# Performance work log

Measured on AMD Instinct MI355X. Metric: run time of the kernel, lower is better.

## Reference

```python
import jax, jax.numpy as jnp
import numpy as np

N_NODES = 10000

def rgcn_layer(x, edge_index, basis, comp, root, bias):
    # x: [N, Fin]; edge_index: [R, 2, E] int; basis: [B, Fin, Fout]; comp: [R, B]
    R, _, E = edge_index.shape
    N = x.shape[0]
    src = edge_index[:, 0]  # [R, E]
    dst = edge_index[:, 1]  # [R, E]
    # basis-decomposed per-relation weights: W_r = sum_b comp[r,b] * basis[b]
    W = jnp.einsum('rb,bio->rio', comp, basis)          # [R, Fin, Fout]
    x_src = x[src]                                       # [R, E, Fin] gather
    msg = jnp.einsum('rei,rio->reo', x_src, W)           # [R, E, Fout]
    # per-relation mean aggregation onto destination nodes
    seg = (jnp.arange(R, dtype=dst.dtype)[:, None] * N + dst).reshape(-1)  # [R*E]
    agg = jax.ops.segment_sum(msg.reshape(R * E, -1), seg, num_segments=R * N)
    deg = jax.ops.segment_sum(jnp.ones((R * E,), x.dtype), seg, num_segments=R * N)
    agg = agg / jnp.maximum(deg, 1.0)[:, None]
    agg = agg.reshape(R, N, -1).sum(0)                   # sum over relations
    return agg + x @ root + bias


def setup_inputs() -> dict:
    key = jax.random.key(0)
    ks = jax.random.split(key, 10)
    s = 0.05  # scale params for numerical sanity
    return {
        'x_drug': jax.random.normal(ks[0], (N_NODES, 2048), jnp.float32),
        'drug_w': jax.random.normal(ks[1], (2048, 128), jnp.float32) * s,
        'edge_index': jax.random.randint(ks[2], (100, 2, 5000), 0, N_NODES, jnp.int32),
        'basis1': jax.random.normal(ks[3], (8, 128, 64), jnp.float32) * s,
        'comp1': jax.random.normal(ks[4], (100, 8), jnp.float32) * s,
        'root1': jax.random.normal(ks[5], (128, 64), jnp.float32) * s,
        'bias1': jnp.zeros((64,), jnp.float32),
        'basis2': jax.random.normal(ks[6], (8, 64, 20), jnp.float32) * s,
        'comp2': jax.random.normal(ks[7], (100, 8), jnp.float32) * s,
        'root2': jax.random.normal(ks[8], (64, 20), jnp.float32) * s,
        'bias2': jnp.zeros((20,), jnp.float32),
    }


def reference(x_drug, drug_w, edge_index, basis1, comp1, root1, bias1,
              basis2, comp2, root2, bias2):
    x = x_drug @ drug_w                                   # dense projection [N, 128]
    h = rgcn_layer(x, edge_index, basis1, comp1, root1, bias1)   # [N, 64]
    h = jax.nn.relu(h)
    out = rgcn_layer(h, edge_index, basis2, comp2, root2, bias2)  # [N, 20]
    return out
```

## Files before the change

### kernel.cpp

```cpp
#include <hip/hip_runtime.h>

#define NN 10000
#define RR 100
#define EE 5000
#define D0 2048
#define D1 128
#define D2 64
#define D3 20
#define NE (RR*EE)
#define MAXD 128

using short8  = __attribute__((ext_vector_type(8))) short;
using float4e = __attribute__((ext_vector_type(4))) float;

typedef const __attribute__((address_space(1))) void g_void;
typedef __attribute__((address_space(3))) void l_void;

__device__ __forceinline__ unsigned short f2bf(float f) {
  unsigned int u = __float_as_uint(f);
  unsigned int r = u + 0x7fffu + ((u >> 16) & 1u);
  return (unsigned short)(r >> 16);
}
__device__ __forceinline__ float bf2f(unsigned short u) {
  return __uint_as_float(((unsigned int)u) << 16);
}
__device__ __forceinline__ unsigned int pk2(float lo, float hi) {
  return ((unsigned int)f2bf(hi) << 16) | (unsigned int)f2bf(lo);
}

#define ZBLK 977
#define CURB 10
#define WTBLK 1024
#define W1BLK 288
#define W2BLK 72
__global__ __launch_bounds__(256) void prep_kernel(
    const float* __restrict__ W, const float* __restrict__ root1,
    const float* __restrict__ basis1, const float* __restrict__ root2,
    const float* __restrict__ basis2, int4* __restrict__ deg4,
    int4* __restrict__ cur4,
    unsigned short* __restrict__ Btw, unsigned short* __restrict__ Wc1T,
    unsigned short* __restrict__ Wc2T) {
  const int b = blockIdx.x, tid = threadIdx.x;
  if (b < ZBLK) {
    int i = b * 256 + tid;
    if (i < (NN * RR) / 4) deg4[i] = make_int4(0, 0, 0, 0);
  } else if (b < ZBLK + CURB) {
    int i = (b - ZBLK) * 256 + tid;
    if (i < 2504) cur4[i] = make_int4(0, 0, 0, 0);
  } else if (b < ZBLK + CURB + WTBLK) {
    int idx = (b - ZBLK - CURB) * 256 + tid;
    int n = idx >> 11, k = idx & 2047;
    Btw[idx] = f2bf(W[(size_t)k * 128 + n]);
  } else if (b < ZBLK + CURB + WTBLK + W1BLK) {
    int idx = (b - ZBLK - CURB - WTBLK) * 256 + tid;
    int o = idx / 1152, j = idx - o * 1152;
    float v = (j < 128) ? root1[j * 64 + o] : basis1[(j - 128) * 64 + o];
    Wc1T[idx] = f2bf(v);
  } else {
    int idx = (b - ZBLK - CURB - WTBLK - W1BLK) * 256 + tid;
    int c = idx / 576, j = idx - c * 576;
    float v = 0.f;
    if (c < 20) v = (j < 64) ? root2[j * 20 + c] : basis2[(j - 64) * 20 + c];
    Wc2T[idx] = f2bf(v);
  }
}

__global__ void deg_kernel(const int* __restrict__ ei, int* __restrict__ deg) {
  int gid = blockIdx.x * 256 + threadIdx.x;
  if (gid >= NE) return;
  int r = gid / EE, e = gid - r * EE;
  int d = ei[r * 2 * EE + EE + e];
  atomicAdd(&deg[r * NN + d], 1);
}

__global__ void scatter_kernel(const int* __restrict__ ei,
                               const int* __restrict__ deg,
                               int* __restrict__ cur, int* __restrict__ rec,
                               float* __restrict__ esc) {
  int gid = blockIdx.x * 256 + threadIdx.x;
  if (gid >= NE) return;
  int r = gid / EE, e = gid - r * EE;
  int s = ei[r * 2 * EE + e];
  int d = ei[r * 2 * EE + EE + e];
  int p = atomicAdd(&cur[d], 1);
  if (p < MAXD) {
    rec[d * MAXD + p] = (r << 14) | s;
    esc[d * MAXD + p] = 1.0f / fmaxf((float)deg[r * NN + d], 1.0f);
  }
}

__global__ __launch_bounds__(256) void gemm0_mfma(
    const float* __restrict__ A, const unsigned short* __restrict__ Btw,
    unsigned short* __restrict__ xb) {
  __shared__ __align__(16) unsigned short Asb[2][16 * 64];
  __shared__ __align__(16) unsigned short Bsb[2][128 * 64];
  const int tid = threadIdx.x;
  const int m0 = blockIdx.x * 16;
  const int wv = tid >> 6, lane = tid & 63;
  const int lrow = lane & 15, quad = lane >> 4;

  const int ar = tid >> 4, ag = tid & 15;
  const float* Ap = &A[(size_t)(m0 + ar) * D0 + ag * 4];
  const int aw = (ar * 128 + ((ag * 8) ^ ((ar & 7) << 4))) >> 1;

  const int rowB = wv * 32 + (lane >> 3);
  const int gch  = (lane & 7) ^ (lane >> 3);
  const unsigned short* BgBase = &Btw[(size_t)rowB * D0 + gch * 8];
  const int ldsB = wv * 2048;

  float4 a0;

#define G0_LOADB(buf, c)                                                     \
  { _Pragma("unroll")                                                        \
    for (int i = 0; i < 4; i++) {                                            \
      __builtin_amdgcn_global_load_lds(                                      \
          (g_void*)(BgBase + (size_t)i * 8 * D0 + (c) * 64),                 \
          (l_void*)&Bsb[buf][ldsB + i * 512], 16, 0, 0);                     \
    } }

#define G0_LOADA(c)  { a0 = *(const float4*)(Ap + (c) * 64); }

#define G0_STOREA(buf)                                                  \
  { uint2 p0;                                                           \
    p0.x = pk2(a0.x, a0.y); p0.y = pk2(a0.z, a0.w);                     \
    *(uint2*)&Asb[buf][aw] = p0; }

#define G0_COMPUTE(buf)                                                 \
  { const int aswz = (lrow & 7) << 4;                                   \
    _Pragma("unroll")                                                   \
    for (int kk = 0; kk < 2; kk++) {                                    \
      short8 af = *(const short8*)&Asb[buf][(lrow * 128 + ((quad * 16 + kk * 64) ^ aswz)) >> 1]; \
      _Pragma("unroll")                                                 \
      for (int nt = 0; nt < 2; nt++) {                                  \
        const int brow = wv * 32 + nt * 16 + lrow;                      \
        short8 bfr = *(const short8*)&Bsb[buf][(brow * 128 + ((quad * 16 + kk * 64) ^ ((brow & 7) << 4))) >> 1]; \
        acc[nt] = __builtin_amdgcn_mfma_f32_16x16x32_bf16(af, bfr, acc[nt], 0, 0, 0); \
      }                                                                 \
    } }

  float4e acc[2];
#pragma unroll
  for (int i = 0; i < 2; i++) { acc[i][0]=0.f; acc[i][1]=0.f; acc[i][2]=0.f; acc[i][3]=0.f; }

  G0_LOADB(0, 0);
  G0_LOADA(0);
  G0_STOREA(0);
  __syncthreads();

#pragma unroll 4
  for (int c = 0; c < 32; c++) {
    if (c < 31) {
      G0_LOADB((c + 1) & 1, c + 1);
      G0_LOADA(c + 1);
      __builtin_amdgcn_sched_barrier(0);
    }
    G0_COMPUTE(c & 1);
    if (c < 31) G0_STOREA((c + 1) & 1);
    __syncthreads();
  }

#pragma unroll
  for (int nt = 0; nt < 2; nt++) {
    const int col = wv * 32 + nt * 16 + lrow;
#pragma unroll
    for (int r = 0; r < 4; r++) {
      const int row = m0 + quad * 4 + r;
      xb[(size_t)row * D1 + col] = f2bf(acc[nt][r]);
    }
  }
}

__global__ __launch_bounds__(256) void agg1e_kernel(
    const unsigned short* __restrict__ xb, const int* __restrict__ cur,
    const int* __restrict__ rec, const float* __restrict__ esc,
    const float* __restrict__ comp, unsigned short* __restrict__ A1b) {
  __shared__ float s_comp[RR * 8];
  const int tid = threadIdx.x;
  for (int i = tid; i < RR * 8; i += 256) s_comp[i] = comp[i];
  __syncthreads();
  const int wv = tid >> 6, lane = tid & 63;
  const int n = blockIdx.x * 4 + wv;
  if (n >= NN) return;
  float acc[8][2];
#pragma unroll
  for (int b = 0; b < 8; b++) { acc[b][0] = 0.f; acc[b][1] = 0.f; }
  int cnt = cur[n]; if (cnt > MAXD) cnt = MAXD;
  const int beg = n * MAXD, end = beg + cnt;
  int idx = beg;
  for (; idx + 3 < end; idx += 4) {
    int rc[4]; float sc[4]; unsigned int xv[4];
#pragma unroll
    for (int u = 0; u < 4; u++) {
      rc[u] = rec[idx + u];
      sc[u] = esc[idx + u];
    }
#pragma unroll
    for (int u = 0; u < 4; u++)
      xv[u] = *(const unsigned int*)&xb[(size_t)(rc[u] & 16383) * D1 + lane * 2];
#pragma unroll
    for (int u = 0; u < 4; u++) {
      const float* cb = &s_comp[(rc[u] >> 14) * 8];
      float x0 = __uint_as_float((xv[u] & 0xffffu) << 16);
      float x1 = __uint_as_float(xv[u] & 0xffff0000u);
#pragma unroll
      for (int b = 0; b < 8; b++) {
        float w = sc[u] * cb[b];
        acc[b][0] += w * x0;
        acc[b][1] += w * x1;
      }
    }
  }
  for (; idx < end; idx++) {
    int rc = rec[idx];
    float sc = esc[idx];
    unsigned int xv = *(const unsigned int*)&xb[(size_t)(rc & 16383) * D1 + lane * 2];
    const float* cb = &s_comp[(rc >> 14) * 8];
    float x0 = __uint_as_float((xv & 0xffffu) << 16);
    float x1 = __uint_as_float(xv & 0xffff0000u);
#pragma unroll
    for (int b = 0; b < 8; b++) {
      float w = sc * cb[b];
      acc[b][0] += w * x0;
      acc[b][1] += w * x1;
    }
  }
#pragma unroll
  for (int b = 0; b < 8; b++) {
    ushort2 o; o.x = f2bf(acc[b][0]); o.y = f2bf(acc[b][1]);
    *(ushort2*)&A1b[(size_t)n * 1024 + b * 128 + lane * 2] = o;
  }
}

__global__ __launch_bounds__(256) void agg2e_kernel(
    const unsigned short* __restrict__ hb, const int* __restrict__ cur,
    const int* __restrict__ rec, const float* __restrict__ esc,
    const float* __restrict__ comp, unsigned short* __restrict__ A2b) {
  __shared__ float s_comp[RR * 8];
  const int tid = threadIdx.x;
  for (int i = tid; i < RR * 8; i += 256) s_comp[i] = comp[i];
  __syncthreads();
  const int wv = tid >> 6, lane = tid & 63;
  const int n = blockIdx.x * 4 + wv;
  if (n >= NN) return;
  float acc[8];
#pragma unroll
  for (int b = 0; b < 8; b++) acc[b] = 0.f;
  int cnt = cur[n]; if (cnt > MAXD) cnt = MAXD;
  const int beg = n * MAXD, end = beg + cnt;
  int idx = beg;
  for (; idx + 3 < end; idx += 4) {
    int rc[4]; float sc[4]; float hv[4];
#pragma unroll
    for (int u = 0; u < 4; u++) {
      rc[u] = rec[idx + u];
      sc[u] = esc[idx + u];
    }
#pragma unroll
    for (int u = 0; u < 4; u++)
      hv[u] = bf2f(hb[(size_t)(rc[u] & 16383) * D2 + lane]);
#pragma unroll
    for (int u = 0; u < 4; u++) {
      const float* cb = &s_comp[(rc[u] >> 14) * 8];
#pragma unroll
      for (int b = 0; b < 8; b++) acc[b] += sc[u] * cb[b] * hv[u];
    }
  }
  for (; idx < end; idx++) {
    int rc = rec[idx];
    float sc = esc[idx];
    float hv = bf2f(hb[(size_t)(rc & 16383) * D2 + lane]);
    const float* cb = &s_comp[(rc >> 14) * 8];
#pragma unroll
    for (int b = 0; b < 8; b++) acc[b] += sc * cb[b] * hv;
  }
#pragma unroll
  for (int b = 0; b < 8; b++)
    A2b[(size_t)n * 512 + b * 64 + lane] = f2bf(acc[b]);
}

__global__ __launch_bounds__(256) void hlayer_mfma(
    const unsigned short* __restrict__ xb, const unsigned short* __restrict__ A1b,
    const unsigned short* __restrict__ Wt, const float* __restrict__ bias1,
    unsigned short* __restrict__ hb) {
  __shared__ __align__(16) unsigned short Asb[2][32 * 64];
  __shared__ __align__(16) unsigned short Bsb[2][64 * 64];
  const int tid = threadIdx.x;
  const int m0 = blockIdx.x * 32;
  const int wv = tid >> 6, lane = tid & 63;
  const int lrow = lane & 15, quad = lane >> 4;
  const int mt = wv >> 1, nb = wv & 1;

  const int ar = tid >> 3, ac = tid & 7;
  int gr = m0 + ar; if (gr >= NN) gr = NN - 1;
  const unsigned short* Ax = &xb[(size_t)gr * D1 + ac * 8];
  const unsigned short* Aa = &A1b[(size_t)gr * 1024 + ac * 8];
  const int asw = (ar & 7) << 4;
  const int aw = (ar * 128 + ((ac * 16) ^ asw)) >> 1;

  const int br = tid >> 2, bq = tid & 3;
  const unsigned short* Bp = &Wt[(size_t)br * 1152 + bq * 16];
  const int bsw = (br & 7) << 4;
  const int bw0 = (br * 128 + ((bq * 32) ^ bsw)) >> 1;
  const int bw1 = (br * 128 + ((bq * 32 + 16) ^ bsw)) >> 1;

  uint4 ra, rb0, rb1;

#define H_LOADG(c)                                                       \
  { int kb = (c) * 64;                                                   \
    ra  = (kb < 128) ? *(const uint4*)(Ax + kb)                          \
                     : *(const uint4*)(Aa + (kb - 128));                 \
    rb0 = *(const uint4*)(Bp + kb);                                      \
    rb1 = *(const uint4*)(Bp + kb + 8); }

#define H_STOREL(buf)                                                    \
  { *(uint4*)&Asb[buf][aw]  = ra;                                        \
    *(uint4*)&Bsb[buf][bw0] = rb0;                                       \
    *(uint4*)&Bsb[buf][bw1] = rb1; }

#define H_COMPUTE(buf)                                                   \
  { const int arow = mt * 16 + lrow;                                     \
    const int aswz = (arow & 7) << 4;                                    \
    _Pragma("unroll")                                                    \
    for (int kk = 0; kk < 2; kk++) {                                     \
      short8 af = *(const short8*)&Asb[buf][(arow * 128 + ((quad * 16 + kk * 64) ^ aswz)) >> 1]; \
      _Pragma("unroll")                                                  \
      for (int nt = 0; nt < 2; nt++) {                                   \
        const int brow = nb * 32 + nt * 16 + lrow;                       \
        short8 bfr = *(const short8*)&Bsb[buf][(brow * 128 + ((quad * 16 + kk * 64) ^ ((brow & 7) << 4))) >> 1]; \
        acc[nt] = __builtin_amdgcn_mfma_f32_16x16x32_bf16(af, bfr, acc[nt], 0, 0, 0); \
      }                                                                  \
    } }

  float4e acc[2];
#pragma unroll
  for (int i = 0; i < 2; i++) { acc[i][0]=0.f; acc[i][1]=0.f; acc[i][2]=0.f; acc[i][3]=0.f; }

  H_LOADG(0);
  H_STOREL(0);
  __syncthreads();

#pragma unroll
  for (int c = 0; c < 18; c++) {
    if (c < 17) {
      H_LOADG(c + 1);
      __builtin_amdgcn_sched_barrier(0);
    }
    H_COMPUTE(c & 1);
    if (c < 17) H_STOREL((c + 1) & 1);
    __syncthreads();
  }

#pragma unroll
  for (int nt = 0; nt < 2; nt++) {
    int col = nb * 32 + nt * 16 + lrow;
    float bv = bias1[col];
#pragma unroll
    for (int r = 0; r < 4; r++) {
      int row = m0 + mt * 16 + quad * 4 + r;
      if (row < NN)
        hb[(size_t)row * D2 + col] = f2bf(fmaxf(acc[nt][r] + bv, 0.f));
    }
  }
}

__global__ __launch_bounds__(256) void out_mfma(
    const unsigned short* __restrict__ hb, const unsigned short* __restrict__ A2b,
    const unsigned short* __restrict__ Wt, const float* __restrict__ bias2,
    float* __restrict__ out) {
  __shared__ __align__(16) unsigned short Asb[2][32 * 64];
  __shared__ __align__(16) unsigned short Bsb[2][32 * 64];
  const int tid = threadIdx.x;
  const int m0 = blockIdx.x * 32;
  const int wv = tid >> 6, lane = tid & 63;
  const int lrow = lane & 15, quad = lane >> 4;
  const int mt = wv >> 1, ntn = wv & 1;

  const int ar = tid >> 3, ac = tid & 7;
  int gr = m0 + ar; if (gr >= NN) gr = NN - 1;
  const unsigned short* Ah = &hb[(size_t)gr * D2 + ac * 8];
  const unsigned short* Aa = &A2b[(size_t)gr * 512 + ac * 8];
  const unsigned short* Bp = &Wt[(size_t)ar * 576 + ac * 8];
  const int asw = (ar & 7) << 4;
  const int aw = (ar * 128 + ((ac * 16) ^ asw)) >> 1;

  uint4 ra, rb;

#define O_LOADG(c)                                                       \
  { int kb = (c) * 64;                                                   \
    ra = (kb < 64) ? *(const uint4*)(Ah)                                 \
                   : *(const uint4*)(Aa + (kb - 64));                    \
    rb = *(const uint4*)(Bp + kb); }

#define O_STOREL(buf)                                                    \
  { *(uint4*)&Asb[buf][aw] = ra;                                         \
    *(uint4*)&Bsb[buf][aw] = rb; }

#define O_COMPUTE(buf)                                                   \
  { const int arow = mt * 16 + lrow;                                     \
    const int aswz = (arow & 7) << 4;                                    \
    const int brow = ntn * 16 + lrow;                                    \
    const int bswz = (brow & 7) << 4;                                    \
    _Pragma("unroll")                                                    \
    for (int kk = 0; kk < 2; kk++) {                                     \
      short8 af = *(const short8*)&Asb[buf][(arow * 128 + ((quad * 16 + kk * 64) ^ aswz)) >> 1]; \
      short8 bfr = *(const short8*)&Bsb[buf][(brow * 128 + ((quad * 16 + kk * 64) ^ bswz)) >> 1]; \
      acc = __builtin_amdgcn_mfma_f32_16x16x32_bf16(af, bfr, acc, 0, 0, 0); \
    } }

  float4e acc;
  acc[0]=0.f; acc[1]=0.f; acc[2]=0.f; acc[3]=0.f;

  O_LOADG(0);
  O_STOREL(0);
  __syncthreads();

#pragma unroll
  for (int c = 0; c < 9; c++) {
    if (c < 8) {
      O_LOADG(c + 1);
      __builtin_amdgcn_sched_barrier(0);
    }
    O_COMPUTE(c & 1);
    if (c < 8) O_STOREL((c + 1) & 1);
    __syncthreads();
  }

  int col = ntn * 16 + lrow;
  if (col < D3) {
    float bv = bias2[col];
#pragma unroll
    for (int r = 0; r < 4; r++) {
      int row = m0 + mt * 16 + quad * 4 + r;
      if (row < NN)
        out[(size_t)row * D3 + col] = acc[r] + bv;
    }
  }
}

extern "C" void kernel_launch(void* const* d_in, const int* in_sizes, int n_in,
                              void* d_out, int out_size, void* d_ws,
                              size_t ws_size, hipStream_t stream) {
  const float* x_drug = (const float*)d_in[0];
  const float* drug_w = (const float*)d_in[1];
  const int*   ei     = (const int*)d_in[2];
  const float* basis1 = (const float*)d_in[3];
  const float* comp1  = (const float*)d_in[4];
  const float* root1  = (const float*)d_in[5];
  const float* bias1  = (const float*)d_in[6];
  const float* basis2 = (const float*)d_in[7];
  const float* comp2  = (const float*)d_in[8];
  const float* root2  = (const float*)d_in[9];
  const float* bias2  = (const float*)d_in[10];
  float* out = (float*)d_out;

  float* ws = (float*)d_ws;
  int*   deg  = (int*)ws;
  int*   cur  = deg + 1000000;
  int*   rec  = cur + 10016;
  float* esc  = (float*)(rec + NN * MAXD);
  unsigned short* xb   = (unsigned short*)(esc + NN * MAXD);
  unsigned short* hb   = (unsigned short*)((float*)xb + 640000);
  unsigned short* Btw  = (unsigned short*)((float*)hb + 320000);
  unsigned short* Wc1T = (unsigned short*)((float*)Btw + 131072);
  unsigned short* Wc2T = (unsigned short*)((float*)Wc1T + 36864);
  float* R1 = (float*)Wc2T + 9216;
  unsigned short* A1b = (unsigned short*)R1;
  unsigned short* A2b = (unsigned short*)R1;

  prep_kernel<<<ZBLK + CURB + WTBLK + W1BLK + W2BLK, 256, 0, stream>>>(
      drug_w, root1, basis1, root2, basis2, (int4*)deg, (int4*)cur,
      Btw, Wc1T, Wc2T);

  deg_kernel<<<(NE + 255) / 256, 256, 0, stream>>>(ei, deg);
  scatter_kernel<<<(NE + 255) / 256, 256, 0, stream>>>(ei, deg, cur, rec, esc);

  gemm0_mfma<<<NN / 16, 256, 0, stream>>>(x_drug, Btw, xb);

  agg1e_kernel<<<(NN + 3) / 4, 256, 0, stream>>>(xb, cur, rec, esc, comp1, A1b);
  hlayer_mfma<<<(NN + 31) / 32, 256, 0, stream>>>(xb, A1b, Wc1T, bias1, hb);

  agg2e_kernel<<<(NN + 3) / 4, 256, 0, stream>>>(hb, cur, rec, esc, comp2, A2b);
  out_mfma<<<(NN + 31) / 32, 256, 0, stream>>>(hb, A2b, Wc2T, bias2, out);
}
```

Baseline: 172.0 us.

## Compute per-relation degrees from per-node edge lists instead of global atomics

Drops the 4 MB dense per-relation degree array, its zeroing blocks and the separate degree-counting kernel. A new finalize kernel builds a per-node histogram of relation ids in shared memory from the already bucketed edge records and writes the inverse degree for each edge. This removes one pass of global atomics and a large memset in exchange for one extra small kernel. Correctness now depends on the MAXD cap, since edges past the cap are no longer counted in the degree.

```diff
diff --git a/kernel.cpp b/kernel.cpp
--- a/kernel.cpp
+++ b/kernel.cpp
@@ -28,7 +28,6 @@
   return ((unsigned int)f2bf(hi) << 16) | (unsigned int)f2bf(lo);
 }
 
-#define ZBLK 977
 #define CURB 10
 #define WTBLK 1024
 #define W1BLK 288
@@ -36,28 +35,24 @@
 __global__ __launch_bounds__(256) void prep_kernel(
     const float* __restrict__ W, const float* __restrict__ root1,
     const float* __restrict__ basis1, const float* __restrict__ root2,
-    const float* __restrict__ basis2, int4* __restrict__ deg4,
-    int4* __restrict__ cur4,
+    const float* __restrict__ basis2, int4* __restrict__ cur4,
     unsigned short* __restrict__ Btw, unsigned short* __restrict__ Wc1T,
     unsigned short* __restrict__ Wc2T) {
   const int b = blockIdx.x, tid = threadIdx.x;
-  if (b < ZBLK) {
+  if (b < CURB) {
     int i = b * 256 + tid;
-    if (i < (NN * RR) / 4) deg4[i] = make_int4(0, 0, 0, 0);
-  } else if (b < ZBLK + CURB) {
-    int i = (b - ZBLK) * 256 + tid;
     if (i < 2504) cur4[i] = make_int4(0, 0, 0, 0);
-  } else if (b < ZBLK + CURB + WTBLK) {
-    int idx = (b - ZBLK - CURB) * 256 + tid;
+  } else if (b < CURB + WTBLK) {
+    int idx = (b - CURB) * 256 + tid;
     int n = idx >> 11, k = idx & 2047;
     Btw[idx] = f2bf(W[(size_t)k * 128 + n]);
-  } else if (b < ZBLK + CURB + WTBLK + W1BLK) {
-    int idx = (b - ZBLK - CURB - WTBLK) * 256 + tid;
+  } else if (b < CURB + WTBLK + W1BLK) {
+    int idx = (b - CURB - WTBLK) * 256 + tid;
     int o = idx / 1152, j = idx - o * 1152;
     float v = (j < 128) ? root1[j * 64 + o] : basis1[(j - 128) * 64 + o];
     Wc1T[idx] = f2bf(v);
   } else {
-    int idx = (b - ZBLK - CURB - WTBLK - W1BLK) * 256 + tid;
+    int idx = (b - CURB - WTBLK - W1BLK) * 256 + tid;
     int c = idx / 576, j = idx - c * 576;
     float v = 0.f;
     if (c < 20) v = (j < 64) ? root2[j * 20 + c] : basis2[(j - 64) * 20 + c];
@@ -65,28 +60,39 @@
   }
 }
 
-__global__ void deg_kernel(const int* __restrict__ ei, int* __restrict__ deg) {
-  int gid = blockIdx.x * 256 + threadIdx.x;
-  if (gid >= NE) return;
-  int r = gid / EE, e = gid - r * EE;
-  int d = ei[r * 2 * EE + EE + e];
-  atomicAdd(&deg[r * NN + d], 1);
-}
-
 __global__ void scatter_kernel(const int* __restrict__ ei,
-                               const int* __restrict__ deg,
-                               int* __restrict__ cur, int* __restrict__ rec,
-                               float* __restrict__ esc) {
+                               int* __restrict__ cur, int* __restrict__ rec) {
   int gid = blockIdx.x * 256 + threadIdx.x;
   if (gid >= NE) return;
   int r = gid / EE, e = gid - r * EE;
   int s = ei[r * 2 * EE + e];
   int d = ei[r * 2 * EE + EE + e];
   int p = atomicAdd(&cur[d], 1);
-  if (p < MAXD) {
-    rec[d * MAXD + p] = (r << 14) | s;
-    esc[d * MAXD + p] = 1.0f / fmaxf((float)deg[r * NN + d], 1.0f);
-  }
+  if (p < MAXD) rec[d * MAXD + p] = (r << 14) | s;
+}
+
+__global__ __launch_bounds__(256) void finalize_kernel(
+    const int* __restrict__ cur, const int* __restrict__ rec,
+    float* __restrict__ esc) {
+  __shared__ int hist[4][RR];
+  const int tid = threadIdx.x;
+  const int wv = tid >> 6, lane = tid & 63;
+  const int n = blockIdx.x * 4 + wv;
+  for (int i = lane; i < RR; i += 64) hist[wv][i] = 0;
+  __syncthreads();
+  int cnt = cur[n]; if (cnt > MAXD) cnt = MAXD;
+  int r0 = 0, r1 = 0;
+  if (lane < cnt) {
+    r0 = rec[n * MAXD + lane] >> 14;
+    atomicAdd(&hist[wv][r0], 1);
+  }
+  if (lane + 64 < cnt) {
+    r1 = rec[n * MAXD + lane + 64] >> 14;
+    atomicAdd(&hist[wv][r1], 1);
+  }
+  __syncthreads();
+  if (lane < cnt)      esc[n * MAXD + lane]      = 1.0f / (float)hist[wv][r0];
+  if (lane + 64 < cnt) esc[n * MAXD + lane + 64] = 1.0f / (float)hist[wv][r1];
 }
 
 __global__ __launch_bounds__(256) void gemm0_mfma(
@@ -454,8 +460,7 @@
   float* out = (float*)d_out;
 
   float* ws = (float*)d_ws;
-  int*   deg  = (int*)ws;
-  int*   cur  = deg + 1000000;
+  int*   cur  = (int*)ws;
   int*   rec  = cur + 10016;
   float* esc  = (float*)(rec + NN * MAXD);
   unsigned short* xb   = (unsigned short*)(esc + NN * MAXD);
@@ -467,12 +472,11 @@
   unsigned short* A1b = (unsigned short*)R1;
   unsigned short* A2b = (unsigned short*)R1;
 
-  prep_kernel<<<ZBLK + CURB + WTBLK + W1BLK + W2BLK, 256, 0, stream>>>(
-      drug_w, root1, basis1, root2, basis2, (int4*)deg, (int4*)cur,
-      Btw, Wc1T, Wc2T);
-
-  deg_kernel<<<(NE + 255) / 256, 256, 0, stream>>>(ei, deg);
-  scatter_kernel<<<(NE + 255) / 256, 256, 0, stream>>>(ei, deg, cur, rec, esc);
+  prep_kernel<<<CURB + WTBLK + W1BLK + W2BLK, 256, 0, stream>>>(
+      drug_w, root1, basis1, root2, basis2, (int4*)cur, Btw, Wc1T, Wc2T);
+
+  scatter_kernel<<<(NE + 255) / 256, 256, 0, stream>>>(ei, cur, rec);
+  finalize_kernel<<<NN / 4, 256, 0, stream>>>(cur, rec, esc);
 
   gemm0_mfma<<<NN / 16, 256, 0, stream>>>(x_drug, Btw, xb);
 
```

After: 152.0 us. 1.13x faster.
